# Kernel tuning notes

Measured on AMD Instinct MI355X. Metric: run time of the kernel, lower is better.

The kernel has to match this reference:

```python
import jax, jax.numpy as jnp
import numpy as np


def setup_inputs() -> dict:
    key = jax.random.key(0)
    k1, k2 = jax.random.split(key)
    B, N, LENGTH = 2048, 64, 8
    # x: (batch, 2, n, n) -- real/imag planes of batched complex matrices
    x = jax.random.normal(k1, (B, 2, N, N), dtype=jnp.float32) * 0.1
    # learned coefficients: (length, 2, n, n), scaled down like the factorial-decaying init
    coefficients = jax.random.normal(k2, (LENGTH, 2, N, N), dtype=jnp.float32) * 0.05
    return {"x": x, "coefficients": coefficients}


def reference(x, coefficients):
    # Faithful port of MatrixMPowerSeriesLayer.call (including the sign used
    # for res_imag inside the i>=2 loop, which differs from the i==1 term).
    length = coefficients.shape[0]
    n = x.shape[2]
    xr = x[:, 0]  # (b, n, n)
    xi = x[:, 1]
    cr = coefficients[:, 0]  # (length, n, n)
    ci = coefficients[:, 1]
    unit = jnp.eye(n, dtype=x.dtype)

    tr, ti = xr, xi  # running complex power x^p
    # order-0 term: unit @ c[0] (broadcasts against batched terms)
    res_r = unit @ cr[0] + (jnp.einsum('bjk,kl->bjl', tr, cr[1]) - jnp.einsum('bjk,kl->bjl', ti, ci[1]))
    res_i = unit @ ci[0] + (jnp.einsum('bjk,kl->bjl', tr, ci[1]) + jnp.einsum('bjk,kl->bjl', ti, cr[1]))

    for i in range(2, length):
        # complex batched matmul: tmp <- tmp @ x
        new_tr = jnp.einsum('bjk,bkl->bjl', tr, xr) - jnp.einsum('bjk,bkl->bjl', ti, xi)
        ti = jnp.einsum('bjk,bkl->bjl', tr, xi) + jnp.einsum('bjk,bkl->bjl', ti, xr)
        tr = new_tr
        res_r = res_r + jnp.einsum('bjk,kl->bjl', tr, cr[i]) - jnp.einsum('bjk,kl->bjl', ti, ci[i])
        # NOTE: original code subtracts ti @ cr[i] here (not adds) -- kept faithful.
        res_i = res_i + jnp.einsum('bjk,kl->bjl', tr, ci[i]) - jnp.einsum('bjk,kl->bjl', ti, cr[i])

    return jnp.stack([res_r, res_i], axis=1)  # (b, 2, n, n)
```

## Files before the change

kernel.cpp:

```cpp
#include <hip/hip_runtime.h>

typedef __attribute__((ext_vector_type(4))) short short4v;
typedef __attribute__((ext_vector_type(8))) short short8v;
typedef __attribute__((ext_vector_type(2))) unsigned int uint2v;
typedef __attribute__((ext_vector_type(4))) unsigned int uint4v;
typedef __attribute__((ext_vector_type(4))) float f32x4;
typedef __attribute__((ext_vector_type(16))) float f32x16;

#define LSTRIDE 68
#define MATB (64 * LSTRIDE * 2)
#define KLDS (6 * MATB)

#define KSLOT_STRIDE 49152
#define CS_OFF (7 * KSLOT_STRIDE)
#define KINIT_OFF (CS_OFF + 2 * 8192)

__device__ __forceinline__ short bf16h(float v) {
    union { float f; unsigned u; } x; x.f = v;
    unsigned r = x.u + 0x7FFFu + ((x.u >> 16) & 1u);
    return (short)(r >> 16);
}
__device__ __forceinline__ float bf16tof(short s) {
    union { unsigned u; float f; } x; x.u = ((unsigned)(unsigned short)s) << 16;
    return x.f;
}
struct HL { unsigned h, l; };
__device__ __forceinline__ HL split2(float v0, float v1) {
    unsigned hp, lp;
    asm("v_cvt_pk_bf16_f32 %0, %1, %2" : "=v"(hp) : "v"(v0), "v"(v1));
    union { unsigned u; float f; } a, b;
    a.u = hp << 16;
    b.u = hp & 0xffff0000u;
    float l0 = v0 - a.f, l1 = v1 - b.f;
    asm("v_cvt_pk_bf16_f32 %0, %1, %2" : "=v"(lp) : "v"(l0), "v"(l1));
    HL r; r.h = hp; r.l = lp; return r;
}
__device__ __forceinline__ f32x16 MF(short8v a, short8v b, f32x16 c) {
    return __builtin_amdgcn_mfma_f32_32x32x16_bf16(a, b, c, 0, 0, 0);
}
__device__ __forceinline__ short8v negf(short8v a) {
    uint4v u = __builtin_bit_cast(uint4v, a);
    u ^= 0x80008000u;
    return __builtin_bit_cast(short8v, u);
}

struct CF { short8v crh, crl, ncih, ncil, cdh, cdl; };
__device__ __forceinline__ CF loadCF(const char* cw, int qr, int lane, int t) {
    CF c;
    c.crh  =      *(const short8v*)(cw + ((size_t)(0 * 2 + qr) * 4 + t) * 1024 + lane * 16);
    c.crl  =      *(const short8v*)(cw + ((size_t)(1 * 2 + qr) * 4 + t) * 1024 + lane * 16);
    c.ncih = negf(*(const short8v*)(cw + ((size_t)(2 * 2 + qr) * 4 + t) * 1024 + lane * 16));
    c.ncil = negf(*(const short8v*)(cw + ((size_t)(3 * 2 + qr) * 4 + t) * 1024 + lane * 16));
    c.cdh  =      *(const short8v*)(cw + ((size_t)(4 * 2 + qr) * 4 + t) * 1024 + lane * 16);
    c.cdl  =      *(const short8v*)(cw + ((size_t)(5 * 2 + qr) * 4 + t) * 1024 + lane * 16);
    return c;
}

__global__ void pms_prep_k(const float* __restrict__ coef, char* __restrict__ wsb) {
    const int blk = blockIdx.x;
    const int lane = threadIdx.x;
    const int lrow = lane & 31, lhi = lane >> 5;
    if (blk < 84) {
        const int s = blk / 12, rem = blk % 12;
        const int mat = rem >> 1, qr = rem & 1;
        const int which = mat >> 1, lo = mat & 1;
        const float* Pr = coef + (size_t)((s + 1) * 2 + 0) * 4096;
        const float* Pi = coef + (size_t)((s + 1) * 2 + 1) * 4096;
        for (int t = 0; t < 4; ++t) {
            short8v o;
            #pragma unroll
            for (int j = 0; j < 8; ++j) {
                int idx = (16 * t + 8 * lhi + j) * 64 + 32 * qr + lrow;
                float v = (which == 0) ? Pr[idx] : (which == 1) ? Pi[idx] : (Pi[idx] - Pr[idx]);
                short hh = bf16h(v);
                o[j] = lo ? bf16h(v - bf16tof(hh)) : hh;
            }
            *(short8v*)(wsb + (size_t)s * KSLOT_STRIDE + mat * 8192 + qr * 4096 + t * 1024 + lane * 16) = o;
        }
    } else if (blk < 88) {
        const int id = blk - 84;
        const int lo = id >> 1, qr = id & 1;
        const float* Pr = coef + (size_t)(1 * 2 + 0) * 4096;
        const float* Pi = coef + (size_t)(1 * 2 + 1) * 4096;
        for (int t = 0; t < 4; ++t) {
            short8v o;
            #pragma unroll
            for (int j = 0; j < 8; ++j) {
                int idx = (16 * t + 8 * lhi + j) * 64 + 32 * qr + lrow;
                float v = Pr[idx] + Pi[idx];
                short hh = bf16h(v);
                o[j] = lo ? bf16h(v - bf16tof(hh)) : hh;
            }
            *(short8v*)(wsb + CS_OFF + lo * 8192 + qr * 4096 + t * 1024 + lane * 16) = o;
        }
    } else {
        const int id = blk - 88;
        const int qc = id & 1, qr = (id >> 1) & 1, slot = id >> 2;
        float* dst = (float*)(wsb + KINIT_OFF + (size_t)(((slot * 2 + qr) * 2 + qc) * 64 + lane) * 64);
        #pragma unroll
        for (int v = 0; v < 16; ++v) {
            int r = 32 * qr + (v & 3) + 8 * (v >> 2) + 4 * lhi;
            int c = 32 * qc + lrow;
            float c0r = coef[c * 64 + r];
            float c0i = coef[4096 + c * 64 + r];
            dst[v] = (slot == 0) ? c0r : (c0i - c0r);
        }
    }
}

__global__ __launch_bounds__(256, 2) void pms_main_k(
    const float* __restrict__ x, const char* __restrict__ wsb,
    float* __restrict__ out)
{
    extern __shared__ char smem[];
    const int tid  = threadIdx.x;
    const int lane = tid & 63;
    const int w    = tid >> 6;
    const int qr = w >> 1, qc = w & 1;
    const int lrow = lane & 31, lhi = lane >> 5;
    const size_t b = blockIdx.x;
    const float* xb = x + b * 8192;

    #pragma unroll
    for (int s = 0; s < 4; ++s) {
        int f = s * 1024 + tid * 4;
        int m = f >> 6, c = f & 63;
        f32x4 vr = *(const f32x4*)(xb + f);
        f32x4 vi = *(const f32x4*)(xb + 4096 + f);
        HL r01 = split2(vr[0], vr[1]), r23 = split2(vr[2], vr[3]);
        HL i01 = split2(vi[0], vi[1]), i23 = split2(vi[2], vi[3]);
        int off = (m * LSTRIDE + c) * 2;
        uint2v u;
        u[0] = r01.h; u[1] = r23.h; *(uint2v*)(smem + 0 * MATB + off) = u;
        u[0] = r01.l; u[1] = r23.l; *(uint2v*)(smem + 1 * MATB + off) = u;
        u[0] = i01.h; u[1] = i23.h; *(uint2v*)(smem + 2 * MATB + off) = u;
        u[0] = i01.l; u[1] = i23.l; *(uint2v*)(smem + 3 * MATB + off) = u;
    }
    __syncthreads();

    short8v xa[2][2][4];
    #pragma unroll
    for (int pi = 0; pi < 2; ++pi)
    #pragma unroll
    for (int hl = 0; hl < 2; ++hl)
    #pragma unroll
    for (int t = 0; t < 4; ++t) {
        const short* mp = (const short*)(smem + (pi * 2 + hl) * MATB);
        short8v a;
        #pragma unroll
        for (int j = 0; j < 8; ++j)
            a[j] = mp[(16 * t + 8 * lhi + j) * LSTRIDE + 32 * qr + lrow];
        xa[pi][hl][t] = a;
    }

    f32x16 accRr, accQ;
    {
        const f32x4* p0 = (const f32x4*)(wsb + KINIT_OFF + (size_t)(((0 + qr) * 2 + qc) * 64 + lane) * 64);
        #pragma unroll
        for (int g = 0; g < 4; ++g) {
            f32x4 a = p0[g];
            #pragma unroll
            for (int j = 0; j < 4; ++j) { accRr[4 * g + j] = a[j]; accQ[4 * g + j] = 0.f; }
        }
    }

    auto ldB = [&](int mat, int t) -> short8v {
        const short4v* p = (const short4v*)(smem + mat * MATB
                             + (32 * qc + lrow) * (LSTRIDE * 2) + 32 * t + 16 * lhi);
        short4v a = p[0], c4 = p[1];
        short8v r;
        #pragma unroll
        for (int j = 0; j < 4; ++j) { r[j] = a[j]; r[j + 4] = c4[j]; }
        return r;
    };

    auto foldWrite = [&](const f32x16& aTr, const f32x16& aTi) {
        const int c = 32 * qc + lrow;
        #pragma unroll
        for (int g = 0; g < 4; ++g) {
            int rbse = 32 * qr + 8 * g + 4 * lhi;
            int off = (c * LSTRIDE + rbse) * 2;
            float s0 = aTr[4 * g + 0] + aTi[4 * g + 0];
            float s1 = aTr[4 * g + 1] + aTi[4 * g + 1];
            float s2 = aTr[4 * g + 2] + aTi[4 * g + 2];
            float s3 = aTr[4 * g + 3] + aTi[4 * g + 3];
            HL a01 = split2(aTr[4 * g + 0], aTr[4 * g + 1]);
            HL a23 = split2(aTr[4 * g + 2], aTr[4 * g + 3]);
            HL b01 = split2(aTi[4 * g + 0], aTi[4 * g + 1]);
            HL b23 = split2(aTi[4 * g + 2], aTi[4 * g + 3]);
            HL c01 = split2(s0, s1);
            HL c23 = split2(s2, s3);
            uint2v u;
            u[0] = a01.h; u[1] = a23.h; *(uint2v*)(smem + 0 * MATB + off) = u;
            u[0] = a01.l; u[1] = a23.l; *(uint2v*)(smem + 1 * MATB + off) = u;
            u[0] = b01.h; u[1] = b23.h; *(uint2v*)(smem + 2 * MATB + off) = u;
            u[0] = b01.l; u[1] = b23.l; *(uint2v*)(smem + 3 * MATB + off) = u;
            u[0] = c01.h; u[1] = c23.h; *(uint2v*)(smem + 4 * MATB + off) = u;
            u[0] = c01.l; u[1] = c23.l; *(uint2v*)(smem + 5 * MATB + off) = u;
        }
    };

    CF cnxt;

    {
        const char* cw = wsb;
        f32x16 aTr, aTi;
        #pragma unroll
        for (int j = 0; j < 16; ++j) { aTr[j] = 0.f; aTi[j] = 0.f; }
        CF c0 = loadCF(cw, qr, lane, 0);
        short8v Brh = ldB(0, 0), Brl = ldB(1, 0);
        short8v Bih = ldB(2, 0), Bil = ldB(3, 0);
        #pragma unroll
        for (int t = 0; t < 4; ++t) {
            CF c1; short8v Nrh, Nrl, Nih, Nil;
            if (t < 3) {
                c1 = loadCF(cw, qr, lane, t + 1);
                Nrh = ldB(0, t + 1); Nrl = ldB(1, t + 1);
                Nih = ldB(2, t + 1); Nil = ldB(3, t + 1);
            }
            short8v csh = *(const short8v*)(wsb + CS_OFF + ((size_t)(0 * 2 + qr) * 4 + t) * 1024 + lane * 16);
            short8v csl = *(const short8v*)(wsb + CS_OFF + ((size_t)(1 * 2 + qr) * 4 + t) * 1024 + lane * 16);
            short8v nBih = negf(Bih), nBil = negf(Bil);

            __builtin_amdgcn_s_setprio(1);
            accRr = MF(c0.crh, Brh, accRr);
            aTr   = MF(xa[0][0][t], Brh, aTr);
            aTi   = MF(xa[1][0][t], Brh, aTi);
            accQ  = MF(c0.cdh, Brh, accQ);

            accRr = MF(c0.crh, Brl, accRr);
            aTr   = MF(xa[0][0][t], Brl, aTr);
            aTi   = MF(xa[1][0][t], Brl, aTi);
            accQ  = MF(c0.cdh, Brl, accQ);

            accRr = MF(c0.crl, Brh, accRr);
            aTr   = MF(xa[0][1][t], Brh, aTr);
            aTi   = MF(xa[1][1][t], Brh, aTi);
            accQ  = MF(c0.cdl, Brh, accQ);

            accRr = MF(c0.ncih, Bih, accRr);
            aTr   = MF(xa[1][0][t], nBih, aTr);
            aTi   = MF(xa[0][0][t], Bih, aTi);
            accQ  = MF(csh, Bih, accQ);

            accRr = MF(c0.ncih, Bil, accRr);
            aTr   = MF(xa[1][0][t], nBil, aTr);
            aTi   = MF(xa[0][0][t], Bil, aTi);
            accQ  = MF(csh, Bil, accQ);

            accRr = MF(c0.ncil, Bih, accRr);
            aTr   = MF(xa[1][1][t], nBih, aTr);
            aTi   = MF(xa[0][1][t], Bih, aTi);
            accQ  = MF(csl, Bih, accQ);
            __builtin_amdgcn_s_setprio(0);

            if (t < 3) { c0 = c1; Brh = Nrh; Brl = Nrl; Bih = Nih; Bil = Nil; }
        }
        cnxt = loadCF(wsb + (size_t)1 * KSLOT_STRIDE, qr, lane, 0);
        __syncthreads();
        foldWrite(aTr, aTi);
        __syncthreads();
    }

    for (int ks = 1; ks <= 5; ++ks) {
        const char* cw = wsb + (size_t)ks * KSLOT_STRIDE;
        f32x16 aTr, aTi;
        #pragma unroll
        for (int j = 0; j < 16; ++j) { aTr[j] = 0.f; aTi[j] = 0.f; }
        CF c0 = cnxt;
        short8v Brh = ldB(0, 0), Brl = ldB(1, 0);
        short8v Bih = ldB(2, 0), Bil = ldB(3, 0);
        #pragma unroll
        for (int t = 0; t < 4; ++t) {
            CF c1; short8v Nrh, Nrl, Nih, Nil;
            if (t < 3) {
                c1 = loadCF(cw, qr, lane, t + 1);
                Nrh = ldB(0, t + 1); Nrl = ldB(1, t + 1);
                Nih = ldB(2, t + 1); Nil = ldB(3, t + 1);
            }
            short8v Bsh = ldB(4, t), Bsl = ldB(5, t);
            short8v nBih = negf(Bih), nBil = negf(Bil);

            __builtin_amdgcn_s_setprio(1);
            accRr = MF(c0.crh, Brh, accRr);
            aTr   = MF(xa[0][0][t], Brh, aTr);
            aTi   = MF(xa[1][0][t], Brh, aTi);

            accRr = MF(c0.crh, Brl, accRr);
            aTr   = MF(xa[0][0][t], Brl, aTr);
            aTi   = MF(xa[1][0][t], Brl, aTi);

            accRr = MF(c0.crl, Brh, accRr);
            aTr   = MF(xa[0][1][t], Brh, aTr);
            aTi   = MF(xa[1][1][t], Brh, aTi);

            accRr = MF(c0.ncih, Bih, accRr);
            aTr   = MF(xa[1][0][t], nBih, aTr);
            aTi   = MF(xa[0][0][t], Bih, aTi);
            accQ  = MF(c0.cdh, Bsh, accQ);

            accRr = MF(c0.ncih, Bil, accRr);
            aTr   = MF(xa[1][0][t], nBil, aTr);
            aTi   = MF(xa[0][0][t], Bil, aTi);
            accQ  = MF(c0.cdh, Bsl, accQ);

            accRr = MF(c0.ncil, Bih, accRr);
            aTr   = MF(xa[1][1][t], nBih, aTr);
            aTi   = MF(xa[0][1][t], Bih, aTi);
            accQ  = MF(c0.cdl, Bsh, accQ);
            __builtin_amdgcn_s_setprio(0);

            if (t < 3) { c0 = c1; Brh = Nrh; Brl = Nrl; Bih = Nih; Bil = Nil; }
        }
        cnxt = loadCF(wsb + (size_t)(ks + 1) * KSLOT_STRIDE, qr, lane, 0);
        __syncthreads();
        foldWrite(aTr, aTi);
        __syncthreads();
    }

    {
        CF c0 = cnxt;
        const char* cw = wsb + (size_t)6 * KSLOT_STRIDE;
        short8v Brh = ldB(0, 0), Brl = ldB(1, 0);
        short8v Bih = ldB(2, 0), Bil = ldB(3, 0);
        #pragma unroll
        for (int t = 0; t < 4; ++t) {
            CF c1; short8v Nrh, Nrl, Nih, Nil;
            if (t < 3) {
                c1 = loadCF(cw, qr, lane, t + 1);
                Nrh = ldB(0, t + 1); Nrl = ldB(1, t + 1);
                Nih = ldB(2, t + 1); Nil = ldB(3, t + 1);
            }
            short8v Bsh = ldB(4, t), Bsl = ldB(5, t);

            __builtin_amdgcn_s_setprio(1);
            accRr = MF(c0.crh, Brh, accRr);
            accQ  = MF(c0.cdh, Bsh, accQ);
            accRr = MF(c0.crh, Brl, accRr);
            accQ  = MF(c0.cdh, Bsl, accQ);
            accRr = MF(c0.crl, Brh, accRr);
            accQ  = MF(c0.cdl, Bsh, accQ);
            accRr = MF(c0.ncih, Bih, accRr);
            accRr = MF(c0.ncih, Bil, accRr);
            accRr = MF(c0.ncil, Bih, accRr);
            __builtin_amdgcn_s_setprio(0);

            if (t < 3) { c0 = c1; Brh = Nrh; Brl = Nrl; Bih = Nih; Bil = Nil; }
        }
    }

    f32x16 accRi;
    {
        const f32x4* p1 = (const f32x4*)(wsb + KINIT_OFF + (size_t)(((2 + qr) * 2 + qc) * 64 + lane) * 64);
        #pragma unroll
        for (int g = 0; g < 4; ++g) {
            f32x4 d = p1[g];
            #pragma unroll
            for (int j = 0; j < 4; ++j)
                accRi[4 * g + j] = accRr[4 * g + j] + accQ[4 * g + j] + d[j];
        }
    }
    __syncthreads();
    {
        const int c = 32 * qc + lrow;
        #pragma unroll
        for (int g = 0; g < 4; ++g) {
            int rbse = 32 * qr + 8 * g + 4 * lhi;
            f32x4 vr, vi;
            #pragma unroll
            for (int j = 0; j < 4; ++j) { vr[j] = accRr[4 * g + j]; vi[j] = accRi[4 * g + j]; }
            *(f32x4*)(smem + (size_t)(0 * 4352 + c * LSTRIDE + rbse) * 4) = vr;
            *(f32x4*)(smem + (size_t)(1 * 4352 + c * LSTRIDE + rbse) * 4) = vi;
        }
    }
    __syncthreads();
    float* ob = out + b * 8192;
    #pragma unroll
    for (int s = 0; s < 8; ++s) {
        int f = s * 1024 + tid * 4;
        int p = f >> 12, m = (f >> 6) & 63, n = f & 63;
        *(f32x4*)(ob + f) = *(const f32x4*)(smem + (size_t)(p * 4352 + m * LSTRIDE + n) * 4);
    }
}

extern "C" void kernel_launch(void* const* d_in, const int* in_sizes, int n_in,
                              void* d_out, int out_size, void* d_ws, size_t ws_size,
                              hipStream_t stream) {
    const float* x    = (const float*)d_in[0];
    const float* coef = (const float*)d_in[1];
    float* out = (float*)d_out;
    char*  wsb = (char*)d_ws;
    const int B = in_sizes[0] / 8192;

    pms_prep_k<<<96, 64, 0, stream>>>(coef, wsb);
    pms_main_k<<<B, 256, KLDS, stream>>>(x, wsb, out);
}
```

Measured before the change: 178.2 us.

## Split warps into power-producer and coefficient-consumer roles with double-buffered LDS

```diff
diff --git a/kernel.cpp b/kernel.cpp
--- a/kernel.cpp
+++ b/kernel.cpp
@@ -9,7 +9,8 @@
 
 #define LSTRIDE 68
 #define MATB (64 * LSTRIDE * 2)
-#define KLDS (6 * MATB)
+#define TBUF (6 * MATB)
+#define LDSZ (2 * TBUF)
 
 #define KSLOT_STRIDE 49152
 #define CS_OFF (7 * KSLOT_STRIDE)
@@ -108,7 +109,7 @@
     }
 }
 
-__global__ __launch_bounds__(256, 2) void pms_main_k(
+__global__ __launch_bounds__(512, 2) void pms_main_k(
     const float* __restrict__ x, const char* __restrict__ wsb,
     float* __restrict__ out)
 {
@@ -116,56 +117,29 @@
     const int tid  = threadIdx.x;
     const int lane = tid & 63;
     const int w    = tid >> 6;
-    const int qr = w >> 1, qc = w & 1;
+    const int role = w >> 2;
+    const int q    = w & 3;
+    const int qr = q >> 1, qc = q & 1;
     const int lrow = lane & 31, lhi = lane >> 5;
     const size_t b = blockIdx.x;
     const float* xb = x + b * 8192;
 
     #pragma unroll
     for (int s = 0; s < 4; ++s) {
-        int f = s * 1024 + tid * 4;
-        int m = f >> 6, c = f & 63;
-        f32x4 vr = *(const f32x4*)(xb + f);
-        f32x4 vi = *(const f32x4*)(xb + 4096 + f);
-        HL r01 = split2(vr[0], vr[1]), r23 = split2(vr[2], vr[3]);
-        HL i01 = split2(vi[0], vi[1]), i23 = split2(vi[2], vi[3]);
+        int f = s * 2048 + tid * 4;
+        int p = f >> 12, m = (f >> 6) & 63, c = f & 63;
+        f32x4 v = *(const f32x4*)(xb + f);
+        HL a01 = split2(v[0], v[1]);
+        HL a23 = split2(v[2], v[3]);
         int off = (m * LSTRIDE + c) * 2;
         uint2v u;
-        u[0] = r01.h; u[1] = r23.h; *(uint2v*)(smem + 0 * MATB + off) = u;
-        u[0] = r01.l; u[1] = r23.l; *(uint2v*)(smem + 1 * MATB + off) = u;
-        u[0] = i01.h; u[1] = i23.h; *(uint2v*)(smem + 2 * MATB + off) = u;
-        u[0] = i01.l; u[1] = i23.l; *(uint2v*)(smem + 3 * MATB + off) = u;
+        u[0] = a01.h; u[1] = a23.h; *(uint2v*)(smem + (p * 2 + 0) * MATB + off) = u;
+        u[0] = a01.l; u[1] = a23.l; *(uint2v*)(smem + (p * 2 + 1) * MATB + off) = u;
     }
     __syncthreads();
 
-    short8v xa[2][2][4];
-    #pragma unroll
-    for (int pi = 0; pi < 2; ++pi)
-    #pragma unroll
-    for (int hl = 0; hl < 2; ++hl)
-    #pragma unroll
-    for (int t = 0; t < 4; ++t) {
-        const short* mp = (const short*)(smem + (pi * 2 + hl) * MATB);
-        short8v a;
-        #pragma unroll
-        for (int j = 0; j < 8; ++j)
-            a[j] = mp[(16 * t + 8 * lhi + j) * LSTRIDE + 32 * qr + lrow];
-        xa[pi][hl][t] = a;
-    }
-
-    f32x16 accRr, accQ;
-    {
-        const f32x4* p0 = (const f32x4*)(wsb + KINIT_OFF + (size_t)(((0 + qr) * 2 + qc) * 64 + lane) * 64);
-        #pragma unroll
-        for (int g = 0; g < 4; ++g) {
-            f32x4 a = p0[g];
-            #pragma unroll
-            for (int j = 0; j < 4; ++j) { accRr[4 * g + j] = a[j]; accQ[4 * g + j] = 0.f; }
-        }
-    }
-
-    auto ldB = [&](int mat, int t) -> short8v {
-        const short4v* p = (const short4v*)(smem + mat * MATB
+    auto ldB = [&](int base, int mat, int t) -> short8v {
+        const short4v* p = (const short4v*)(smem + base + mat * MATB
                              + (32 * qc + lrow) * (LSTRIDE * 2) + 32 * t + 16 * lhi);
         short4v a = p[0], c4 = p[1];
         short8v r;
@@ -174,164 +148,179 @@
         return r;
     };
 
-    auto foldWrite = [&](const f32x16& aTr, const f32x16& aTi) {
-        const int c = 32 * qc + lrow;
+    short8v xa[2][2][4];
+    f32x16 accRr, accQ;
+    if (role == 0) {
+        #pragma unroll
+        for (int pi = 0; pi < 2; ++pi)
+        #pragma unroll
+        for (int hl = 0; hl < 2; ++hl)
+        #pragma unroll
+        for (int t = 0; t < 4; ++t) {
+            const short* mp = (const short*)(smem + (pi * 2 + hl) * MATB);
+            short8v a;
+            #pragma unroll
+            for (int j = 0; j < 8; ++j)
+                a[j] = mp[(16 * t + 8 * lhi + j) * LSTRIDE + 32 * qr + lrow];
+            xa[pi][hl][t] = a;
+        }
+    } else {
+        const f32x4* p0 = (const f32x4*)(wsb + KINIT_OFF + (size_t)(((0 + qr) * 2 + qc) * 64 + lane) * 64);
         #pragma unroll
         for (int g = 0; g < 4; ++g) {
-            int rbse = 32 * qr + 8 * g + 4 * lhi;
-            int off = (c * LSTRIDE + rbse) * 2;
-            float s0 = aTr[4 * g + 0] + aTi[4 * g + 0];
-            float s1 = aTr[4 * g + 1] + aTi[4 * g + 1];
-            float s2 = aTr[4 * g + 2] + aTi[4 * g + 2];
-            float s3 = aTr[4 * g + 3] + aTi[4 * g + 3];
-            HL a01 = split2(aTr[4 * g + 0], aTr[4 * g + 1]);
-            HL a23 = split2(aTr[4 * g + 2], aTr[4 * g + 3]);
-            HL b01 = split2(aTi[4 * g + 0], aTi[4 * g + 1]);
-            HL b23 = split2(aTi[4 * g + 2], aTi[4 * g + 3]);
-            HL c01 = split2(s0, s1);
-            HL c23 = split2(s2, s3);
-            uint2v u;
-            u[0] = a01.h; u[1] = a23.h; *(uint2v*)(smem + 0 * MATB + off) = u;
-            u[0] = a01.l; u[1] = a23.l; *(uint2v*)(smem + 1 * MATB + off) = u;
-            u[0] = b01.h; u[1] = b23.h; *(uint2v*)(smem + 2 * MATB + off) = u;
-            u[0] = b01.l; u[1] = b23.l; *(uint2v*)(smem + 3 * MATB + off) = u;
-            u[0] = c01.h; u[1] = c23.h; *(uint2v*)(smem + 4 * MATB + off) = u;
-            u[0] = c01.l; u[1] = c23.l; *(uint2v*)(smem + 5 * MATB + off) = u;
-        }
-    };
-
-    CF cnxt;
-
-    {
-        const char* cw = wsb;
-        f32x16 aTr, aTi;
-        #pragma unroll
-        for (int j = 0; j < 16; ++j) { aTr[j] = 0.f; aTi[j] = 0.f; }
+            f32x4 a = p0[g];
+            #pragma unroll
+            for (int j = 0; j < 4; ++j) { accRr[4 * g + j] = a[j]; accQ[4 * g + j] = 0.f; }
+        }
+    }
+
+    int cur = 0, nxt = TBUF;
+
+    for (int k = 2; k <= 7; ++k) {
+        const char* cw = wsb + (size_t)(k - 2) * KSLOT_STRIDE;
+
+        if (role == 0) {
+            f32x16 aTr, aTi;
+            #pragma unroll
+            for (int j = 0; j < 16; ++j) { aTr[j] = 0.f; aTi[j] = 0.f; }
+            short8v Brh = ldB(cur, 0, 0), Brl = ldB(cur, 1, 0);
+            short8v Bih = ldB(cur, 2, 0), Bil = ldB(cur, 3, 0);
+            #pragma unroll
+            for (int t = 0; t < 4; ++t) {
+                short8v Nrh, Nrl, Nih, Nil;
+                if (t < 3) {
+                    Nrh = ldB(cur, 0, t + 1); Nrl = ldB(cur, 1, t + 1);
+                    Nih = ldB(cur, 2, t + 1); Nil = ldB(cur, 3, t + 1);
+                }
+                short8v nBih = negf(Bih), nBil = negf(Bil);
+
+                __builtin_amdgcn_s_setprio(1);
+                aTr = MF(xa[0][0][t], Brh, aTr);
+                aTi = MF(xa[1][0][t], Brh, aTi);
+                aTr = MF(xa[0][0][t], Brl, aTr);
+                aTi = MF(xa[1][0][t], Brl, aTi);
+                aTr = MF(xa[0][1][t], Brh, aTr);
+                aTi = MF(xa[1][1][t], Brh, aTi);
+                aTr = MF(xa[1][0][t], nBih, aTr);
+                aTi = MF(xa[0][0][t], Bih, aTi);
+                aTr = MF(xa[1][0][t], nBil, aTr);
+                aTi = MF(xa[0][0][t], Bil, aTi);
+                aTr = MF(xa[1][1][t], nBih, aTr);
+                aTi = MF(xa[0][1][t], Bih, aTi);
+                __builtin_amdgcn_s_setprio(0);
+
+                if (t < 3) { Brh = Nrh; Brl = Nrl; Bih = Nih; Bil = Nil; }
+            }
+            {
+                const int c = 32 * qc + lrow;
+                #pragma unroll
+                for (int g = 0; g < 4; ++g) {
+                    int rbse = 32 * qr + 8 * g + 4 * lhi;
+                    int off = (c * LSTRIDE + rbse) * 2;
+                    float s0 = aTr[4 * g + 0] + aTi[4 * g + 0];
+                    float s1 = aTr[4 * g + 1] + aTi[4 * g + 1];
+                    float s2 = aTr[4 * g + 2] + aTi[4 * g + 2];
+                    float s3 = aTr[4 * g + 3] + aTi[4 * g + 3];
+                    HL a01 = split2(aTr[4 * g + 0], aTr[4 * g + 1]);
+                    HL a23 = split2(aTr[4 * g + 2], aTr[4 * g + 3]);
+                    HL b01 = split2(aTi[4 * g + 0], aTi[4 * g + 1]);
+                    HL b23 = split2(aTi[4 * g + 2], aTi[4 * g + 3]);
+                    HL c01 = split2(s0, s1);
+                    HL c23 = split2(s2, s3);
+                    uint2v u;
+                    u[0] = a01.h; u[1] = a23.h; *(uint2v*)(smem + nxt + 0 * MATB + off) = u;
+                    u[0] = a01.l; u[1] = a23.l; *(uint2v*)(smem + nxt + 1 * MATB + off) = u;
+                    u[0] = b01.h; u[1] = b23.h; *(uint2v*)(smem + nxt + 2 * MATB + off) = u;
+                    u[0] = b01.l; u[1] = b23.l; *(uint2v*)(smem + nxt + 3 * MATB + off) = u;
+                    u[0] = c01.h; u[1] = c23.h; *(uint2v*)(smem + nxt + 4 * MATB + off) = u;
+                    u[0] = c01.l; u[1] = c23.l; *(uint2v*)(smem + nxt + 5 * MATB + off) = u;
+                }
+            }
+        } else if (k == 2) {
+            CF c0 = loadCF(cw, qr, lane, 0);
+            short8v Brh = ldB(cur, 0, 0), Brl = ldB(cur, 1, 0);
+            short8v Bih = ldB(cur, 2, 0), Bil = ldB(cur, 3, 0);
+            #pragma unroll
+            for (int t = 0; t < 4; ++t) {
+                CF c1; short8v Nrh, Nrl, Nih, Nil;
+                if (t < 3) {
+                    c1 = loadCF(cw, qr, lane, t + 1);
+                    Nrh = ldB(cur, 0, t + 1); Nrl = ldB(cur, 1, t + 1);
+                    Nih = ldB(cur, 2, t + 1); Nil = ldB(cur, 3, t + 1);
+                }
+                short8v csh = *(const short8v*)(wsb + CS_OFF + ((size_t)(0 * 2 + qr) * 4 + t) * 1024 + lane * 16);
+                short8v csl = *(const short8v*)(wsb + CS_OFF + ((size_t)(1 * 2 + qr) * 4 + t) * 1024 + lane * 16);
+
+                __builtin_amdgcn_s_setprio(1);
+                accRr = MF(c0.crh, Brh, accRr);
+                accQ  = MF(c0.cdh, Brh, accQ);
+                accRr = MF(c0.crh, Brl, accRr);
+                accQ  = MF(c0.cdh, Brl, accQ);
+                accRr = MF(c0.crl, Brh, accRr);
+                accQ  = MF(c0.cdl, Brh, accQ);
+                accRr = MF(c0.ncih, Bih, accRr);
+                accQ  = MF(csh, Bih, accQ);
+                accRr = MF(c0.ncih, Bil, accRr);
+                accQ  = MF(csh, Bil, accQ);
+                accRr = MF(c0.ncil, Bih, accRr);
+                accQ  = MF(csl, Bih, accQ);
+                __builtin_amdgcn_s_setprio(0);
+
+                if (t < 3) { c0 = c1; Brh = Nrh; Brl = Nrl; Bih = Nih; Bil = Nil; }
+            }
+        } else {
+            CF c0 = loadCF(cw, qr, lane, 0);
+            short8v Brh = ldB(cur, 0, 0), Brl = ldB(cur, 1, 0);
+            short8v Bih = ldB(cur, 2, 0), Bil = ldB(cur, 3, 0);
+            short8v Bsh = ldB(cur, 4, 0), Bsl = ldB(cur, 5, 0);
+            #pragma unroll
+            for (int t = 0; t < 4; ++t) {
+                CF c1; short8v Nrh, Nrl, Nih, Nil, Nsh, Nsl;
+                if (t < 3) {
+                    c1 = loadCF(cw, qr, lane, t + 1);
+                    Nrh = ldB(cur, 0, t + 1); Nrl = ldB(cur, 1, t + 1);
+                    Nih = ldB(cur, 2, t + 1); Nil = ldB(cur, 3, t + 1);
+                    Nsh = ldB(cur, 4, t + 1); Nsl = ldB(cur, 5, t + 1);
+                }
+
+                __builtin_amdgcn_s_setprio(1);
+                accRr = MF(c0.crh, Brh, accRr);
+                accQ  = MF(c0.cdh, Bsh, accQ);
+                accRr = MF(c0.crh, Brl, accRr);
+                accQ  = MF(c0.cdh, Bsl, accQ);
+                accRr = MF(c0.crl, Brh, accRr);
+                accQ  = MF(c0.cdl, Bsh, accQ);
+                accRr = MF(c0.ncih, Bih, accRr);
+                accRr = MF(c0.ncih, Bil, accRr);
+                accRr = MF(c0.ncil, Bih, accRr);
+                __builtin_amdgcn_s_setprio(0);
+
+                if (t < 3) {
+                    c0 = c1; Brh = Nrh; Brl = Nrl; Bih = Nih; Bil = Nil;
+                    Bsh = Nsh; Bsl = Nsl;
+                }
+            }
+        }
+
+        __syncthreads();
+        int tmp = cur; cur = nxt; nxt = tmp;
+    }
+
+    if (role == 1) {
+        const char* cw = wsb + (size_t)6 * KSLOT_STRIDE;
         CF c0 = loadCF(cw, qr, lane, 0);
-        short8v Brh = ldB(0, 0), Brl = ldB(1, 0);
-        short8v Bih = ldB(2, 0), Bil = ldB(3, 0);
+        short8v Brh = ldB(cur, 0, 0), Brl = ldB(cur, 1, 0);
+        short8v Bih = ldB(cur, 2, 0), Bil = ldB(cur, 3, 0);
+        short8v Bsh = ldB(cur, 4, 0), Bsl = ldB(cur, 5, 0);
         #pragma unroll
         for (int t = 0; t < 4; ++t) {
-            CF c1; short8v Nrh, Nrl, Nih, Nil;
+            CF c1; short8v Nrh, Nrl, Nih, Nil, Nsh, Nsl;
             if (t < 3) {
                 c1 = loadCF(cw, qr, lane, t + 1);
-                Nrh = ldB(0, t + 1); Nrl = ldB(1, t + 1);
-                Nih = ldB(2, t + 1); Nil = ldB(3, t + 1);
-            }
-            short8v csh = *(const short8v*)(wsb + CS_OFF + ((size_t)(0 * 2 + qr) * 4 + t) * 1024 + lane * 16);
-            short8v csl = *(const short8v*)(wsb + CS_OFF + ((size_t)(1 * 2 + qr) * 4 + t) * 1024 + lane * 16);
-            short8v nBih = negf(Bih), nBil = negf(Bil);
-
-            __builtin_amdgcn_s_setprio(1);
-            accRr = MF(c0.crh, Brh, accRr);
-            aTr   = MF(xa[0][0][t], Brh, aTr);
-            aTi   = MF(xa[1][0][t], Brh, aTi);
-            accQ  = MF(c0.cdh, Brh, accQ);
-
-            accRr = MF(c0.crh, Brl, accRr);
-            aTr   = MF(xa[0][0][t], Brl, aTr);
-            aTi   = MF(xa[1][0][t], Brl, aTi);
-            accQ  = MF(c0.cdh, Brl, accQ);
-
-            accRr = MF(c0.crl, Brh, accRr);
-            aTr   = MF(xa[0][1][t], Brh, aTr);
-            aTi   = MF(xa[1][1][t], Brh, aTi);
-            accQ  = MF(c0.cdl, Brh, accQ);
-
-            accRr = MF(c0.ncih, Bih, accRr);
-            aTr   = MF(xa[1][0][t], nBih, aTr);
-            aTi   = MF(xa[0][0][t], Bih, aTi);
-            accQ  = MF(csh, Bih, accQ);
-
-            accRr = MF(c0.ncih, Bil, accRr);
-            aTr   = MF(xa[1][0][t], nBil, aTr);
-            aTi   = MF(xa[0][0][t], Bil, aTi);
-            accQ  = MF(csh, Bil, accQ);
-
-            accRr = MF(c0.ncil, Bih, accRr);
-            aTr   = MF(xa[1][1][t], nBih, aTr);
-            aTi   = MF(xa[0][1][t], Bih, aTi);
-            accQ  = MF(csl, Bih, accQ);
-            __builtin_amdgcn_s_setprio(0);
-
-            if (t < 3) { c0 = c1; Brh = Nrh; Brl = Nrl; Bih = Nih; Bil = Nil; }
-        }
-        cnxt = loadCF(wsb + (size_t)1 * KSLOT_STRIDE, qr, lane, 0);
-        __syncthreads();
-        foldWrite(aTr, aTi);
-        __syncthreads();
-    }
-
-    for (int ks = 1; ks <= 5; ++ks) {
-        const char* cw = wsb + (size_t)ks * KSLOT_STRIDE;
-        f32x16 aTr, aTi;
-        #pragma unroll
-        for (int j = 0; j < 16; ++j) { aTr[j] = 0.f; aTi[j] = 0.f; }
-        CF c0 = cnxt;
-        short8v Brh = ldB(0, 0), Brl = ldB(1, 0);
-        short8v Bih = ldB(2, 0), Bil = ldB(3, 0);
-        #pragma unroll
-        for (int t = 0; t < 4; ++t) {
-            CF c1; short8v Nrh, Nrl, Nih, Nil;
-            if (t < 3) {
-                c1 = loadCF(cw, qr, lane, t + 1);
-                Nrh = ldB(0, t + 1); Nrl = ldB(1, t + 1);
-                Nih = ldB(2, t + 1); Nil = ldB(3, t + 1);
-            }
-            short8v Bsh = ldB(4, t), Bsl = ldB(5, t);
-            short8v nBih = negf(Bih), nBil = negf(Bil);
-
-            __builtin_amdgcn_s_setprio(1);
-            accRr = MF(c0.crh, Brh, accRr);
-            aTr   = MF(xa[0][0][t], Brh, aTr);
-            aTi   = MF(xa[1][0][t], Brh, aTi);
-
-            accRr = MF(c0.crh, Brl, accRr);
-            aTr   = MF(xa[0][0][t], Brl, aTr);
-            aTi   = MF(xa[1][0][t], Brl, aTi);
-
-            accRr = MF(c0.crl, Brh, accRr);
-            aTr   = MF(xa[0][1][t], Brh, aTr);
-            aTi   = MF(xa[1][1][t], Brh, aTi);
-
-            accRr = MF(c0.ncih, Bih, accRr);
-            aTr   = MF(xa[1][0][t], nBih, aTr);
-            aTi   = MF(xa[0][0][t], Bih, aTi);
-            accQ  = MF(c0.cdh, Bsh, accQ);
-
-            accRr = MF(c0.ncih, Bil, accRr);
-            aTr   = MF(xa[1][0][t], nBil, aTr);
-            aTi   = MF(xa[0][0][t], Bil, aTi);
-            accQ  = MF(c0.cdh, Bsl, accQ);
-
-            accRr = MF(c0.ncil, Bih, accRr);
-            aTr   = MF(xa[1][1][t], nBih, aTr);
-            aTi   = MF(xa[0][1][t], Bih, aTi);
-            accQ  = MF(c0.cdl, Bsh, accQ);
-            __builtin_amdgcn_s_setprio(0);
-
-            if (t < 3) { c0 = c1; Brh = Nrh; Brl = Nrl; Bih = Nih; Bil = Nil; }
-        }
-        cnxt = loadCF(wsb + (size_t)(ks + 1) * KSLOT_STRIDE, qr, lane, 0);
-        __syncthreads();
-        foldWrite(aTr, aTi);
-        __syncthreads();
-    }
-
-    {
-        CF c0 = cnxt;
-        const char* cw = wsb + (size_t)6 * KSLOT_STRIDE;
-        short8v Brh = ldB(0, 0), Brl = ldB(1, 0);
-        short8v Bih = ldB(2, 0), Bil = ldB(3, 0);
-        #pragma unroll
-        for (int t = 0; t < 4; ++t) {
-            CF c1; short8v Nrh, Nrl, Nih, Nil;
-            if (t < 3) {
-                c1 = loadCF(cw, qr, lane, t + 1);
-                Nrh = ldB(0, t + 1); Nrl = ldB(1, t + 1);
-                Nih = ldB(2, t + 1); Nil = ldB(3, t + 1);
-            }
-            short8v Bsh = ldB(4, t), Bsl = ldB(5, t);
+                Nrh = ldB(cur, 0, t + 1); Nrl = ldB(cur, 1, t + 1);
+                Nih = ldB(cur, 2, t + 1); Nil = ldB(cur, 3, t + 1);
+                Nsh = ldB(cur, 4, t + 1); Nsl = ldB(cur, 5, t + 1);
+            }
 
             __builtin_amdgcn_s_setprio(1);
             accRr = MF(c0.crh, Brh, accRr);
@@ -345,39 +334,39 @@
             accRr = MF(c0.ncil, Bih, accRr);
             __builtin_amdgcn_s_setprio(0);
 
-            if (t < 3) { c0 = c1; Brh = Nrh; Brl = Nrl; Bih = Nih; Bil = Nil; }
-        }
-    }
-
-    f32x16 accRi;
-    {
+            if (t < 3) {
+                c0 = c1; Brh = Nrh; Brl = Nrl; Bih = Nih; Bil = Nil;
+                Bsh = Nsh; Bsl = Nsl;
+            }
+        }
+    }
+
+    __syncthreads();
+
+    if (role == 1) {
         const f32x4* p1 = (const f32x4*)(wsb + KINIT_OFF + (size_t)(((2 + qr) * 2 + qc) * 64 + lane) * 64);
+        const int c = 32 * qc + lrow;
         #pragma unroll
         for (int g = 0; g < 4; ++g) {
             f32x4 d = p1[g];
-            #pragma unroll
-            for (int j = 0; j < 4; ++j)
-                accRi[4 * g + j] = accRr[4 * g + j] + accQ[4 * g + j] + d[j];
-        }
-    }
-    __syncthreads();
-    {
-        const int c = 32 * qc + lrow;
-        #pragma unroll
-        for (int g = 0; g < 4; ++g) {
             int rbse = 32 * qr + 8 * g + 4 * lhi;
             f32x4 vr, vi;
             #pragma unroll
-            for (int j = 0; j < 4; ++j) { vr[j] = accRr[4 * g + j]; vi[j] = accRi[4 * g + j]; }
+            for (int j = 0; j < 4; ++j) {
+                float rr = accRr[4 * g + j];
+                vr[j] = rr;
+                vi[j] = rr + accQ[4 * g + j] + d[j];
+            }
             *(f32x4*)(smem + (size_t)(0 * 4352 + c * LSTRIDE + rbse) * 4) = vr;
             *(f32x4*)(smem + (size_t)(1 * 4352 + c * LSTRIDE + rbse) * 4) = vi;
         }
     }
     __syncthreads();
+
     float* ob = out + b * 8192;
     #pragma unroll
-    for (int s = 0; s < 8; ++s) {
-        int f = s * 1024 + tid * 4;
+    for (int s = 0; s < 4; ++s) {
+        int f = s * 2048 + tid * 4;
         int p = f >> 12, m = (f >> 6) & 63, n = f & 63;
         *(f32x4*)(ob + f) = *(const f32x4*)(smem + (size_t)(p * 4352 + m * LSTRIDE + n) * 4);
     }
@@ -392,6 +381,9 @@
     char*  wsb = (char*)d_ws;
     const int B = in_sizes[0] / 8192;
 
+    (void)hipFuncSetAttribute(reinterpret_cast<const void*>(&pms_main_k),
+                              hipFuncAttributeMaxDynamicSharedMemorySize, LDSZ);
+
     pms_prep_k<<<96, 64, 0, stream>>>(coef, wsb);
-    pms_main_k<<<B, 256, KLDS, stream>>>(x, wsb, out);
-}
+    pms_main_k<<<B, 512, LDSZ, stream>>>(x, wsb, out);
+}
```

Measured after the change: 232.9 us. +30.7%, slower.
